# Performance work log

Measured on AMD Instinct MI355X. Metric: run time of the kernel, lower is better.

The kernel has to match this reference:

```python
import jax, jax.numpy as jnp
import numpy as np


def setup_inputs() -> dict:
    key = jax.random.key(0)
    ks = jax.random.split(key, 8)
    B, S, D, H = 32, 8192, 256, 256  # batch, seq_len, input_dim, hidden_dim
    bound = 1.0 / np.sqrt(H)
    x = jax.random.normal(ks[0], (B, H), dtype=jnp.float32)
    context = jax.random.normal(ks[1], (B, S, D), dtype=jnp.float32)
    mask = jax.random.randint(ks[2], (B, S), 0, 2, dtype=jnp.int32)
    # input_linear: Linear(H, H)
    W_in = jax.random.uniform(ks[3], (H, H), jnp.float32, -bound, bound)
    b_in = jax.random.uniform(ks[4], (H,), jnp.float32, -bound, bound)
    # context_linear: Conv1d(D, H, kernel=1) == pointwise linear over features
    W_ctx = jax.random.uniform(ks[5], (H, D), jnp.float32, -1.0 / np.sqrt(D), 1.0 / np.sqrt(D))
    b_ctx = jax.random.uniform(ks[6], (H,), jnp.float32, -1.0 / np.sqrt(D), 1.0 / np.sqrt(D))
    V = jax.random.uniform(ks[7], (H,), jnp.float32, -bound, bound)
    return {"x": x, "context": context, "mask": mask,
            "W_in": W_in, "b_in": b_in, "W_ctx": W_ctx, "b_ctx": b_ctx, "V": V}


def reference(x, context, mask, W_in, b_in, W_ctx, b_ctx, V):
    # inp: [B, H] -> broadcast over seq as [B, 1, H]
    inp = (x @ W_in.T + b_in)[:, None, :]
    # ctx: Conv1d(kernel=1) over permuted context == per-position linear: [B, S, H]
    ctx = jnp.einsum('bsd,hd->bsh', context, W_ctx) + b_ctx
    # score: V . tanh(inp + ctx) reduced over H -> [B, S]
    att = jnp.einsum('bsh,h->bs', jnp.tanh(inp + ctx), V)
    att = 10.0 * jnp.tanh(att)
    att = jnp.where(mask.astype(bool), att, -jnp.inf)
    ans = jax.nn.softmax(att, axis=1)
    indices = jnp.argmax(ans, axis=1)
    p = jnp.max(ans, axis=1)
    return (indices, p[:, None], mask.astype(bool))
```

## Files before the change

kernel.cpp:

```cpp
#include <hip/hip_runtime.h>
#include <math.h>

#define S_LEN 8192
#define BATCH 32
#define HDIM 256
#define DDIM 256
#define TS 64
#define LDK 264

typedef float f32x4 __attribute__((ext_vector_type(4)));
typedef short s16x8 __attribute__((ext_vector_type(8)));
typedef short s16x4 __attribute__((ext_vector_type(4)));

static __device__ __forceinline__ unsigned short bf16_rne(float f) {
    unsigned u = __float_as_uint(f);
    u += 0x7FFFu + ((u >> 16) & 1u);
    return (unsigned short)(u >> 16);
}
static __device__ __forceinline__ float bf16_f32(unsigned short h) {
    return __uint_as_float(((unsigned)h) << 16);
}
static __device__ __forceinline__ float fast_tanh(float x) {
    float e = __expf(2.0f * x);
    return 1.0f - 2.0f / (e + 1.0f);
}

__global__ void prep_kernel(const float* __restrict__ x,
                            const float* __restrict__ W_in,
                            const float* __restrict__ b_in,
                            const float* __restrict__ W_ctx,
                            const float* __restrict__ b_ctx,
                            float* __restrict__ cin,
                            unsigned short* __restrict__ Wf_hi,
                            unsigned short* __restrict__ Wf_lo) {
    __shared__ float xs[DDIM];
    const int bx = blockIdx.x;
    const int t  = threadIdx.x;
    if (bx < BATCH) {
        xs[t] = x[bx * DDIM + t];
        __syncthreads();
        const float* wr = W_in + t * DDIM;
        float acc = b_in[t] + b_ctx[t];
        #pragma unroll 8
        for (int d = 0; d < DDIM; ++d) acc += xs[d] * wr[d];
        cin[bx * HDIM + t] = acc;
    } else {
        const int g  = (bx - BATCH) * 256 + t;
        const int nt = g >> 9;
        const int ks = (g >> 6) & 7;
        const int l  = g & 63;
        const int h  = nt * 16 + (l & 15);
        const int d0 = ks * 32 + (l >> 4) * 8;
        const float* src = W_ctx + h * DDIM + d0;
        s16x8 vh, vl;
        #pragma unroll
        for (int j = 0; j < 8; ++j) {
            float f = src[j];
            unsigned short hb = bf16_rne(f);
            vh[j] = (short)hb;
            vl[j] = (short)bf16_rne(f - bf16_f32(hb));
        }
        *(s16x8*)(Wf_hi + (size_t)g * 8) = vh;
        *(s16x8*)(Wf_lo + (size_t)g * 8) = vl;
    }
}

__launch_bounds__(256, 2)
__global__ void att_kernel(const float* __restrict__ context,
                           const int* __restrict__ mask,
                           const float* __restrict__ cin,
                           const float* __restrict__ V,
                           const unsigned short* __restrict__ Wf_hi,
                           const unsigned short* __restrict__ Wf_lo,
                           float* __restrict__ att,
                           float* __restrict__ out_mask) {
    __shared__ unsigned short a_hi[TS * LDK];
    __shared__ unsigned short a_lo[TS * LDK];
    __shared__ float cin_s[HDIM];
    __shared__ float v_s[HDIM];
    __shared__ float att_part[4][TS];

    const int sblk = blockIdx.x;
    const int b    = blockIdx.y;
    const int t    = threadIdx.x;
    const int w    = t >> 6;
    const int l    = t & 63;
    const int lane16 = l & 15;
    const int q      = l >> 4;

    cin_s[t] = cin[b * HDIM + t];
    v_s[t]   = V[t];

    const float* cbase = context + ((size_t)b * S_LEN + (size_t)sblk * TS) * DDIM;
    #pragma unroll
    for (int i = 0; i < 16; ++i) {
        int f   = i * 256 + t;
        int row = f >> 6;
        int c4  = f & 63;
        f32x4 v = *(const f32x4*)(cbase + row * DDIM + c4 * 4);
        s16x4 hi, lo;
        #pragma unroll
        for (int j = 0; j < 4; ++j) {
            unsigned short hb = bf16_rne(v[j]);
            hi[j] = (short)hb;
            lo[j] = (short)bf16_rne(v[j] - bf16_f32(hb));
        }
        *(s16x4*)(a_hi + row * LDK + c4 * 4) = hi;
        *(s16x4*)(a_lo + row * LDK + c4 * 4) = lo;
    }
    __syncthreads();

    f32x4 acc[4][4];
    #pragma unroll
    for (int mt = 0; mt < 4; ++mt)
        #pragma unroll
        for (int i = 0; i < 4; ++i) acc[mt][i] = (f32x4){0.f, 0.f, 0.f, 0.f};

    const int ntb = w * 4;
    for (int ks = 0; ks < 8; ++ks) {
        s16x8 bh[4], bl[4];
        #pragma unroll
        for (int i = 0; i < 4; ++i) {
            size_t off = ((size_t)((ntb + i) * 8 + ks) * 64 + l) * 8;
            bh[i] = *(const s16x8*)(Wf_hi + off);
            bl[i] = *(const s16x8*)(Wf_lo + off);
        }
        s16x8 ah[4], al[4];
        #pragma unroll
        for (int mt = 0; mt < 4; ++mt) {
            int o = (mt * 16 + lane16) * LDK + ks * 32 + q * 8;
            ah[mt] = *(const s16x8*)(a_hi + o);
            al[mt] = *(const s16x8*)(a_lo + o);
        }
        #pragma unroll
        for (int mt = 0; mt < 4; ++mt)
            #pragma unroll
            for (int i = 0; i < 4; ++i) {
                acc[mt][i] = __builtin_amdgcn_mfma_f32_16x16x32_bf16(ah[mt], bh[i], acc[mt][i], 0, 0, 0);
                acc[mt][i] = __builtin_amdgcn_mfma_f32_16x16x32_bf16(ah[mt], bl[i], acc[mt][i], 0, 0, 0);
                acc[mt][i] = __builtin_amdgcn_mfma_f32_16x16x32_bf16(al[mt], bh[i], acc[mt][i], 0, 0, 0);
            }
    }

    float part[4][4] = {};
    #pragma unroll
    for (int i = 0; i < 4; ++i) {
        int h = (ntb + i) * 16 + lane16;
        float c  = cin_s[h];
        float vv = v_s[h];
        #pragma unroll
        for (int mt = 0; mt < 4; ++mt)
            #pragma unroll
            for (int r = 0; r < 4; ++r)
                part[mt][r] += fast_tanh(acc[mt][i][r] + c) * vv;
    }
    #pragma unroll
    for (int mt = 0; mt < 4; ++mt)
        #pragma unroll
        for (int r = 0; r < 4; ++r) {
            float v = part[mt][r];
            v += __shfl_xor(v, 1);
            v += __shfl_xor(v, 2);
            v += __shfl_xor(v, 4);
            v += __shfl_xor(v, 8);
            part[mt][r] = v;
        }
    if (lane16 == 0) {
        #pragma unroll
        for (int mt = 0; mt < 4; ++mt)
            #pragma unroll
            for (int r = 0; r < 4; ++r)
                att_part[w][mt * 16 + q * 4 + r] = part[mt][r];
    }
    __syncthreads();

    if (t < TS) {
        float a = att_part[0][t] + att_part[1][t] + att_part[2][t] + att_part[3][t];
        a = 10.0f * fast_tanh(a);
        int s  = sblk * TS + t;
        int mk = mask[b * S_LEN + s];
        att[(size_t)b * S_LEN + s] = mk ? a : -INFINITY;
        out_mask[(size_t)b * S_LEN + s] = mk ? 1.0f : 0.0f;
    }
}

__global__ void reduce_kernel(const float* __restrict__ att,
                              float* __restrict__ out) {
    __shared__ float smax[256];
    __shared__ int   sidx[256];
    const int b = blockIdx.x;
    const int t = threadIdx.x;
    const float* row = att + (size_t)b * S_LEN;

    float best = -INFINITY;
    int   bid  = 0x7fffffff;
    for (int s = t; s < S_LEN; s += 256) {
        float v = row[s];
        if (v > best) { best = v; bid = s; }
    }
    smax[t] = best; sidx[t] = bid;
    __syncthreads();
    for (int off = 128; off > 0; off >>= 1) {
        if (t < off) {
            float ov = smax[t + off]; int oi = sidx[t + off];
            if (ov > smax[t] || (ov == smax[t] && oi < sidx[t])) { smax[t] = ov; sidx[t] = oi; }
        }
        __syncthreads();
    }
    const float mx = smax[0];
    const int   ix = sidx[0];
    __syncthreads();

    float sum = 0.f;
    for (int s = t; s < S_LEN; s += 256)
        sum += __expf(row[s] - mx);
    smax[t] = sum;
    __syncthreads();
    for (int off = 128; off > 0; off >>= 1) {
        if (t < off) smax[t] += smax[t + off];
        __syncthreads();
    }
    if (t == 0) {
        out[b]         = (float)ix;
        out[BATCH + b] = 1.0f / smax[0];
    }
}

extern "C" void kernel_launch(void* const* d_in, const int* in_sizes, int n_in,
                              void* d_out, int out_size, void* d_ws, size_t ws_size,
                              hipStream_t stream) {
    const float* x       = (const float*)d_in[0];
    const float* context = (const float*)d_in[1];
    const int*   mask    = (const int*)d_in[2];
    const float* W_in    = (const float*)d_in[3];
    const float* b_in    = (const float*)d_in[4];
    const float* W_ctx   = (const float*)d_in[5];
    const float* b_ctx   = (const float*)d_in[6];
    const float* V       = (const float*)d_in[7];
    float* out = (float*)d_out;

    char* ws = (char*)d_ws;
    float*          cin   = (float*)ws;
    unsigned short* Wf_hi = (unsigned short*)(ws + 32 * 1024);
    unsigned short* Wf_lo = (unsigned short*)(ws + 160 * 1024);
    float*          att   = (float*)(ws + 288 * 1024);

    float* out_mask = out + 64;

    prep_kernel<<<64, 256, 0, stream>>>(x, W_in, b_in, W_ctx, b_ctx, cin, Wf_hi, Wf_lo);
    dim3 grid(S_LEN / TS, BATCH);
    att_kernel<<<grid, 256, 0, stream>>>(context, mask, cin, V, Wf_hi, Wf_lo, att, out_mask);
    reduce_kernel<<<BATCH, 256, 0, stream>>>(att, out);
}
```

Measured before the change: 460.5 us.

## Switch split-bf16 GEMM to fp16 with two MFMAs and smaller tiles

The context projection moves from a three-term bf16 hi/lo split to fp16. Context is still split into hi and lo halves, but W_ctx is stored as a single fp16 copy, so each tile needs two MFMAs instead of three and half as many weight loads. The sequence tile shrinks from 64 to 32 rows and the launch bounds rise to 4 blocks per CU, aiming for more occupancy and latency hiding. The single fp16 weight copy and round-toward-zero conversions lower precision, which could flip argmax ties near the top score. fp16 range limits are unlikely to matter for these inputs.

```diff
diff --git a/kernel.cpp b/kernel.cpp
--- a/kernel.cpp
+++ b/kernel.cpp
@@ -5,21 +5,15 @@
 #define BATCH 32
 #define HDIM 256
 #define DDIM 256
-#define TS 64
+#define TS 32
 #define LDK 264
 
 typedef float f32x4 __attribute__((ext_vector_type(4)));
-typedef short s16x8 __attribute__((ext_vector_type(8)));
-typedef short s16x4 __attribute__((ext_vector_type(4)));
-
-static __device__ __forceinline__ unsigned short bf16_rne(float f) {
-    unsigned u = __float_as_uint(f);
-    u += 0x7FFFu + ((u >> 16) & 1u);
-    return (unsigned short)(u >> 16);
-}
-static __device__ __forceinline__ float bf16_f32(unsigned short h) {
-    return __uint_as_float(((unsigned)h) << 16);
-}
+typedef __fp16 h16x2 __attribute__((ext_vector_type(2)));
+typedef __fp16 h16x4 __attribute__((ext_vector_type(4)));
+typedef _Float16 f16x4 __attribute__((ext_vector_type(4)));
+typedef _Float16 f16x8 __attribute__((ext_vector_type(8)));
+
 static __device__ __forceinline__ float fast_tanh(float x) {
     float e = __expf(2.0f * x);
     return 1.0f - 2.0f / (e + 1.0f);
@@ -31,8 +25,7 @@
                             const float* __restrict__ W_ctx,
                             const float* __restrict__ b_ctx,
                             float* __restrict__ cin,
-                            unsigned short* __restrict__ Wf_hi,
-                            unsigned short* __restrict__ Wf_lo) {
+                            _Float16* __restrict__ Wf) {
     __shared__ float xs[DDIM];
     const int bx = blockIdx.x;
     const int t  = threadIdx.x;
@@ -52,30 +45,23 @@
         const int h  = nt * 16 + (l & 15);
         const int d0 = ks * 32 + (l >> 4) * 8;
         const float* src = W_ctx + h * DDIM + d0;
-        s16x8 vh, vl;
-        #pragma unroll
-        for (int j = 0; j < 8; ++j) {
-            float f = src[j];
-            unsigned short hb = bf16_rne(f);
-            vh[j] = (short)hb;
-            vl[j] = (short)bf16_rne(f - bf16_f32(hb));
-        }
-        *(s16x8*)(Wf_hi + (size_t)g * 8) = vh;
-        *(s16x8*)(Wf_lo + (size_t)g * 8) = vl;
-    }
-}
-
-__launch_bounds__(256, 2)
+        f16x8 vh;
+        #pragma unroll
+        for (int j = 0; j < 8; ++j) vh[j] = (_Float16)src[j];
+        *(f16x8*)(Wf + (size_t)g * 8) = vh;
+    }
+}
+
+__launch_bounds__(256, 4)
 __global__ void att_kernel(const float* __restrict__ context,
                            const int* __restrict__ mask,
                            const float* __restrict__ cin,
                            const float* __restrict__ V,
-                           const unsigned short* __restrict__ Wf_hi,
-                           const unsigned short* __restrict__ Wf_lo,
+                           const _Float16* __restrict__ Wf,
                            float* __restrict__ att,
                            float* __restrict__ out_mask) {
-    __shared__ unsigned short a_hi[TS * LDK];
-    __shared__ unsigned short a_lo[TS * LDK];
+    __shared__ _Float16 a_hi[TS * LDK];
+    __shared__ _Float16 a_lo[TS * LDK];
     __shared__ float cin_s[HDIM];
     __shared__ float v_s[HDIM];
     __shared__ float att_part[4][TS];
@@ -93,69 +79,67 @@
 
     const float* cbase = context + ((size_t)b * S_LEN + (size_t)sblk * TS) * DDIM;
     #pragma unroll
-    for (int i = 0; i < 16; ++i) {
+    for (int i = 0; i < 8; ++i) {
         int f   = i * 256 + t;
         int row = f >> 6;
         int c4  = f & 63;
         f32x4 v = *(const f32x4*)(cbase + row * DDIM + c4 * 4);
-        s16x4 hi, lo;
-        #pragma unroll
-        for (int j = 0; j < 4; ++j) {
-            unsigned short hb = bf16_rne(v[j]);
-            hi[j] = (short)hb;
-            lo[j] = (short)bf16_rne(v[j] - bf16_f32(hb));
-        }
-        *(s16x4*)(a_hi + row * LDK + c4 * 4) = hi;
-        *(s16x4*)(a_lo + row * LDK + c4 * 4) = lo;
-    }
-    __syncthreads();
-
-    f32x4 acc[4][4];
-    #pragma unroll
-    for (int mt = 0; mt < 4; ++mt)
+        h16x2 h0 = __builtin_amdgcn_cvt_pkrtz(v[0], v[1]);
+        h16x2 h1 = __builtin_amdgcn_cvt_pkrtz(v[2], v[3]);
+        h16x2 l0 = __builtin_amdgcn_cvt_pkrtz(v[0] - (float)h0[0], v[1] - (float)h0[1]);
+        h16x2 l1 = __builtin_amdgcn_cvt_pkrtz(v[2] - (float)h1[0], v[3] - (float)h1[1]);
+        h16x4 hi; hi[0] = h0[0]; hi[1] = h0[1]; hi[2] = h1[0]; hi[3] = h1[1];
+        h16x4 lo; lo[0] = l0[0]; lo[1] = l0[1]; lo[2] = l1[0]; lo[3] = l1[1];
+        *(h16x4*)(a_hi + row * LDK + c4 * 4) = hi;
+        *(h16x4*)(a_lo + row * LDK + c4 * 4) = lo;
+    }
+    __syncthreads();
+
+    f32x4 acc[2][4];
+    #pragma unroll
+    for (int mt = 0; mt < 2; ++mt)
         #pragma unroll
         for (int i = 0; i < 4; ++i) acc[mt][i] = (f32x4){0.f, 0.f, 0.f, 0.f};
 
     const int ntb = w * 4;
+    #pragma unroll
     for (int ks = 0; ks < 8; ++ks) {
-        s16x8 bh[4], bl[4];
+        f16x8 bh[4];
         #pragma unroll
         for (int i = 0; i < 4; ++i) {
-            size_t off = ((size_t)((ntb + i) * 8 + ks) * 64 + l) * 8;
-            bh[i] = *(const s16x8*)(Wf_hi + off);
-            bl[i] = *(const s16x8*)(Wf_lo + off);
-        }
-        s16x8 ah[4], al[4];
-        #pragma unroll
-        for (int mt = 0; mt < 4; ++mt) {
+            int off = (((ntb + i) * 8 + ks) * 64 + l) * 8;
+            bh[i] = *(const f16x8*)(Wf + off);
+        }
+        f16x8 ah[2], al[2];
+        #pragma unroll
+        for (int mt = 0; mt < 2; ++mt) {
             int o = (mt * 16 + lane16) * LDK + ks * 32 + q * 8;
-            ah[mt] = *(const s16x8*)(a_hi + o);
-            al[mt] = *(const s16x8*)(a_lo + o);
-        }
-        #pragma unroll
-        for (int mt = 0; mt < 4; ++mt)
+            ah[mt] = *(const f16x8*)(a_hi + o);
+            al[mt] = *(const f16x8*)(a_lo + o);
+        }
+        #pragma unroll
+        for (int mt = 0; mt < 2; ++mt)
             #pragma unroll
             for (int i = 0; i < 4; ++i) {
-                acc[mt][i] = __builtin_amdgcn_mfma_f32_16x16x32_bf16(ah[mt], bh[i], acc[mt][i], 0, 0, 0);
-                acc[mt][i] = __builtin_amdgcn_mfma_f32_16x16x32_bf16(ah[mt], bl[i], acc[mt][i], 0, 0, 0);
-                acc[mt][i] = __builtin_amdgcn_mfma_f32_16x16x32_bf16(al[mt], bh[i], acc[mt][i], 0, 0, 0);
+                acc[mt][i] = __builtin_amdgcn_mfma_f32_16x16x32_f16(ah[mt], bh[i], acc[mt][i], 0, 0, 0);
+                acc[mt][i] = __builtin_amdgcn_mfma_f32_16x16x32_f16(al[mt], bh[i], acc[mt][i], 0, 0, 0);
             }
     }
 
-    float part[4][4] = {};
+    float part[2][4] = {};
     #pragma unroll
     for (int i = 0; i < 4; ++i) {
         int h = (ntb + i) * 16 + lane16;
         float c  = cin_s[h];
         float vv = v_s[h];
         #pragma unroll
-        for (int mt = 0; mt < 4; ++mt)
+        for (int mt = 0; mt < 2; ++mt)
             #pragma unroll
             for (int r = 0; r < 4; ++r)
                 part[mt][r] += fast_tanh(acc[mt][i][r] + c) * vv;
     }
     #pragma unroll
-    for (int mt = 0; mt < 4; ++mt)
+    for (int mt = 0; mt < 2; ++mt)
         #pragma unroll
         for (int r = 0; r < 4; ++r) {
             float v = part[mt][r];
@@ -167,7 +151,7 @@
         }
     if (lane16 == 0) {
         #pragma unroll
-        for (int mt = 0; mt < 4; ++mt)
+        for (int mt = 0; mt < 2; ++mt)
             #pragma unroll
             for (int r = 0; r < 4; ++r)
                 att_part[w][mt * 16 + q * 4 + r] = part[mt][r];
@@ -240,15 +224,14 @@
     float* out = (float*)d_out;
 
     char* ws = (char*)d_ws;
-    float*          cin   = (float*)ws;
-    unsigned short* Wf_hi = (unsigned short*)(ws + 32 * 1024);
-    unsigned short* Wf_lo = (unsigned short*)(ws + 160 * 1024);
-    float*          att   = (float*)(ws + 288 * 1024);
+    float*    cin = (float*)ws;
+    _Float16* Wf  = (_Float16*)(ws + 32 * 1024);
+    float*    att = (float*)(ws + 160 * 1024);
 
     float* out_mask = out + 64;
 
-    prep_kernel<<<64, 256, 0, stream>>>(x, W_in, b_in, W_ctx, b_ctx, cin, Wf_hi, Wf_lo);
+    prep_kernel<<<64, 256, 0, stream>>>(x, W_in, b_in, W_ctx, b_ctx, cin, Wf);
     dim3 grid(S_LEN / TS, BATCH);
-    att_kernel<<<grid, 256, 0, stream>>>(context, mask, cin, V, Wf_hi, Wf_lo, att, out_mask);
+    att_kernel<<<grid, 256, 0, stream>>>(context, mask, cin, V, Wf, att, out_mask);
     reduce_kernel<<<BATCH, 256, 0, stream>>>(att, out);
 }
```

Measured after the change: 434.6 us. -5.6%, faster.
